# Kernel tuning notes

Measured on AMD Instinct MI355X. Metric: run time of the kernel, lower is better.

The kernel has to match this reference:

```python
import jax, jax.numpy as jnp
import numpy as np

B, L, H, R = 8, 8256, 768, 24  # L = 128*129/2 flattened token-pair positions


def setup_inputs() -> dict:
    key = jax.random.key(0)
    k1, k2, k3 = jax.random.split(key, 3)
    hidden_state = jax.random.normal(k1, (B, L, H), dtype=jnp.float32)
    # per-relation Linear(hidden_size, 3) weights, stacked: (R, 3, H), (R, 3)
    W = jax.random.normal(k2, (R, 3, H), dtype=jnp.float32) * 0.02
    b = jax.random.normal(k3, (R, 3), dtype=jnp.float32) * 0.02
    return {"hidden_state": hidden_state, "W": W, "b": b}


def reference(hidden_state, W, b):
    # Batched equivalent of the per-relation Linear loop + stack(dim=1):
    # logits[b, r, l, t] = sum_h hidden_state[b,l,h] * W[r,t,h] + b[r,t]
    logits = jnp.einsum('blh,rth->brlt', hidden_state, W) + b[None, :, None, :]
    return jax.nn.softmax(logits, axis=-1)  # (B, R, L, 3)
```

## Files before the change

kernel.cpp:

```cpp
#include <hip/hip_runtime.h>


#define HD     768
#define LSEQ   8256
#define RREL   24
#define KSTEPS 24
#define NT     5
#define NCOL   72

typedef float f32x4 __attribute__((ext_vector_type(4)));
typedef short s16x8 __attribute__((ext_vector_type(8)));
typedef int   i32x4 __attribute__((ext_vector_type(4)));

__device__ __forceinline__ unsigned f2bf(float f) {
  unsigned u = __builtin_bit_cast(unsigned, f);
  u += 0x7FFFu + ((u >> 16) & 1u);
  return u >> 16;
}
__device__ __forceinline__ int pack2(float lo, float hi) {
  return (int)(f2bf(lo) | (f2bf(hi) << 16));
}

__global__ void conv_w_kernel(const float* __restrict__ W,
                              unsigned short* __restrict__ wsB) {
  int idx = blockIdx.x * 256 + threadIdx.x;
  if (idx >= KSTEPS * NT * 64) return;
  int ks   = idx / (NT * 64);
  int rem  = idx - ks * (NT * 64);
  int nt   = rem >> 6;
  int lane = rem & 63;
  int col  = nt * 16 + (lane & 15);
  int k0   = ks * 32 + (lane >> 4) * 8;
  unsigned short v[8] = {0, 0, 0, 0, 0, 0, 0, 0};
  if (col < NCOL) {
    const float* p = W + (size_t)col * HD + k0;
    float4 a = *(const float4*)p;
    float4 b = *(const float4*)(p + 4);
    v[0] = (unsigned short)f2bf(a.x); v[1] = (unsigned short)f2bf(a.y);
    v[2] = (unsigned short)f2bf(a.z); v[3] = (unsigned short)f2bf(a.w);
    v[4] = (unsigned short)f2bf(b.x); v[5] = (unsigned short)f2bf(b.y);
    v[6] = (unsigned short)f2bf(b.z); v[7] = (unsigned short)f2bf(b.w);
  }
  *(s16x8*)(wsB + (size_t)idx * 8) = *(s16x8*)v;
}

#define ALOAD(ks) do { if ((ks) < KSTEPS) {                        \
    abuf[(ks) % 3][0] = *(const float4*)(pA + (ks) * 32);          \
    abuf[(ks) % 3][1] = *(const float4*)(pA + (ks) * 32 + 4);      \
  } } while (0)

#define BLOAD_WS(ks) do { if ((ks) < KSTEPS) {                     \
    _Pragma("unroll")                                              \
    for (int nt_ = 0; nt_ < NT; ++nt_)                             \
      bbuf[(ks) & 1][nt_] = pWS[(ks) * NT * 64 + nt_ * 64 + lane]; \
  } } while (0)

#define BLOAD_FB(ks) do { if ((ks) < KSTEPS) {                     \
    _Pragma("unroll")                                              \
    for (int nt_ = 0; nt_ < 4; ++nt_) {                            \
      fbf[(ks) & 1][nt_][0] = *(const float4*)(pB[nt_] + (ks)*32); \
      fbf[(ks) & 1][nt_][1] = *(const float4*)(pB[nt_] + (ks)*32 + 4); \
    }                                                              \
    if (b4ok) {                                                    \
      fbf[(ks) & 1][4][0] = *(const float4*)(pB[4] + (ks)*32);     \
      fbf[(ks) & 1][4][1] = *(const float4*)(pB[4] + (ks)*32 + 4); \
    } else {                                                       \
      fbf[(ks) & 1][4][0] = make_float4(0.f,0.f,0.f,0.f);          \
      fbf[(ks) & 1][4][1] = make_float4(0.f,0.f,0.f,0.f);          \
    }                                                              \
  } } while (0)

template <bool USE_WS>
__global__ __launch_bounds__(256, 4)
void tagging_main(const float* __restrict__ hs, const float* __restrict__ W,
                  const float* __restrict__ bias,
                  const i32x4* __restrict__ pWS, float* __restrict__ out) {
  __shared__ float lg[4][16][84];

  const int lane = threadIdx.x & 63;
  const int wid  = threadIdx.x >> 6;
  const int m0   = (blockIdx.x * 4 + wid) * 16;

  const float* pA = hs + (size_t)(m0 + (lane >> 2)) * HD + (lane & 3) * 8;
  const int bp = ((lane & 15) * 4 + (lane >> 4)) * 4;

  const float* pB[NT];
  #pragma unroll
  for (int nt = 0; nt < NT; ++nt)
    pB[nt] = W + (size_t)(nt * 16 + (lane & 15)) * HD + (lane >> 4) * 8;
  const bool b4ok = (lane & 15) < 8;

  f32x4  acc[NT] = {};
  float4 abuf[3][2];
  i32x4  bbuf[2][NT];
  float4 fbf[2][NT][2];

  ALOAD(0); ALOAD(1);
  if constexpr (USE_WS) { BLOAD_WS(0); } else { BLOAD_FB(0); }

  #pragma unroll
  for (int ks = 0; ks < KSTEPS; ++ks) {
    ALOAD(ks + 2);
    if constexpr (USE_WS) { BLOAD_WS(ks + 1); } else { BLOAD_FB(ks + 1); }

    float4 a0 = abuf[ks % 3][0], a1 = abuf[ks % 3][1];
    int d0 = pack2(a0.x, a0.y), d1 = pack2(a0.z, a0.w);
    int d2 = pack2(a1.x, a1.y), d3 = pack2(a1.z, a1.w);
    i32x4 av;
    av[0] = __builtin_amdgcn_ds_bpermute(bp, d0);
    av[1] = __builtin_amdgcn_ds_bpermute(bp, d1);
    av[2] = __builtin_amdgcn_ds_bpermute(bp, d2);
    av[3] = __builtin_amdgcn_ds_bpermute(bp, d3);
    s16x8 af = __builtin_bit_cast(s16x8, av);

    #pragma unroll
    for (int nt = 0; nt < NT; ++nt) {
      s16x8 bf;
      if constexpr (USE_WS) {
        bf = __builtin_bit_cast(s16x8, bbuf[ks & 1][nt]);
      } else {
        float4 b0 = fbf[ks & 1][nt][0], b1 = fbf[ks & 1][nt][1];
        i32x4 bv;
        bv[0] = pack2(b0.x, b0.y); bv[1] = pack2(b0.z, b0.w);
        bv[2] = pack2(b1.x, b1.y); bv[3] = pack2(b1.z, b1.w);
        bf = __builtin_bit_cast(s16x8, bv);
      }
      acc[nt] = __builtin_amdgcn_mfma_f32_16x16x32_bf16(af, bf, acc[nt], 0, 0, 0);
    }
  }

  #pragma unroll
  for (int nt = 0; nt < NT; ++nt)
    #pragma unroll
    for (int j = 0; j < 4; ++j)
      lg[wid][(lane >> 4) * 4 + j][nt * 16 + (lane & 15)] = acc[nt][j];
  __syncthreads();

  #pragma unroll
  for (int it = 0; it < 6; ++it) {
    int flat = it * 64 + lane;
    int g    = flat >> 4;
    int tokl = flat & 15;
    unsigned tok = (unsigned)(m0 + tokl);
    unsigned b   = tok / LSEQ;
    unsigned l   = tok - b * LSEQ;
    float x0 = lg[wid][tokl][3 * g + 0] + bias[3 * g + 0];
    float x1 = lg[wid][tokl][3 * g + 1] + bias[3 * g + 1];
    float x2 = lg[wid][tokl][3 * g + 2] + bias[3 * g + 2];
    float mx = fmaxf(x0, fmaxf(x1, x2));
    float e0 = __expf(x0 - mx), e1 = __expf(x1 - mx), e2 = __expf(x2 - mx);
    float inv = 1.0f / (e0 + e1 + e2);
    size_t o = ((size_t)(b * RREL + g) * LSEQ + l) * 3;
    out[o + 0] = e0 * inv;
    out[o + 1] = e1 * inv;
    out[o + 2] = e2 * inv;
  }
}

extern "C" void kernel_launch(void* const* d_in, const int* in_sizes, int n_in,
                              void* d_out, int out_size, void* d_ws, size_t ws_size,
                              hipStream_t stream) {
  (void)in_sizes; (void)n_in; (void)out_size;
  const float* hs   = (const float*)d_in[0];
  const float* W    = (const float*)d_in[1];
  const float* bias = (const float*)d_in[2];
  float* out = (float*)d_out;

  const size_t needB = (size_t)KSTEPS * NT * 64 * 8 * 2;
  if (d_ws && ws_size >= needB) {
    hipLaunchKernelGGL(conv_w_kernel, dim3(30), dim3(256), 0, stream,
                       W, (unsigned short*)d_ws);
    hipLaunchKernelGGL((tagging_main<true>), dim3(1032), dim3(256), 0, stream,
                       hs, W, bias, (const i32x4*)d_ws, out);
  } else {
    hipLaunchKernelGGL((tagging_main<false>), dim3(1032), dim3(256), 0, stream,
                       hs, W, bias, nullptr, out);
  }
}
```

Measured before the change: 52.64 us.

## Use single-wave blocks computing two 16-row M tiles to reuse B fragments

Each block becomes one 64-thread wave that computes 32 tokens as two 16-row MFMA tiles, so every B fragment load feeds two MFMAs. The per-token batch division in the epilogue is hoisted to one per block, and the bf16 packing switches to the HIP intrinsic conversion. This roughly halves the weight-fragment traffic per token and drops the multi-wave block structure. In exchange it doubles accumulator and A-buffer registers, and with 64-thread blocks there may be fewer resident waves per CU.

```diff
diff --git a/kernel.cpp b/kernel.cpp
--- a/kernel.cpp
+++ b/kernel.cpp
@@ -1,4 +1,5 @@
 #include <hip/hip_runtime.h>
+#include <hip/hip_bf16.h>
 
 
 #define HD     768
@@ -12,13 +13,16 @@
 typedef short s16x8 __attribute__((ext_vector_type(8)));
 typedef int   i32x4 __attribute__((ext_vector_type(4)));
 
-__device__ __forceinline__ unsigned f2bf(float f) {
+__device__ __forceinline__ unsigned f2bf_rne(float f) {
   unsigned u = __builtin_bit_cast(unsigned, f);
   u += 0x7FFFu + ((u >> 16) & 1u);
   return u >> 16;
 }
+
 __device__ __forceinline__ int pack2(float lo, float hi) {
-  return (int)(f2bf(lo) | (f2bf(hi) << 16));
+  unsigned l = __bfloat16_as_ushort(__float2bfloat16(lo));
+  unsigned h = __bfloat16_as_ushort(__float2bfloat16(hi));
+  return (int)(l | (h << 16));
 }
 
 __global__ void conv_w_kernel(const float* __restrict__ W,
@@ -36,17 +40,20 @@
     const float* p = W + (size_t)col * HD + k0;
     float4 a = *(const float4*)p;
     float4 b = *(const float4*)(p + 4);
-    v[0] = (unsigned short)f2bf(a.x); v[1] = (unsigned short)f2bf(a.y);
-    v[2] = (unsigned short)f2bf(a.z); v[3] = (unsigned short)f2bf(a.w);
-    v[4] = (unsigned short)f2bf(b.x); v[5] = (unsigned short)f2bf(b.y);
-    v[6] = (unsigned short)f2bf(b.z); v[7] = (unsigned short)f2bf(b.w);
+    v[0] = (unsigned short)f2bf_rne(a.x); v[1] = (unsigned short)f2bf_rne(a.y);
+    v[2] = (unsigned short)f2bf_rne(a.z); v[3] = (unsigned short)f2bf_rne(a.w);
+    v[4] = (unsigned short)f2bf_rne(b.x); v[5] = (unsigned short)f2bf_rne(b.y);
+    v[6] = (unsigned short)f2bf_rne(b.z); v[7] = (unsigned short)f2bf_rne(b.w);
   }
   *(s16x8*)(wsB + (size_t)idx * 8) = *(s16x8*)v;
 }
 
 #define ALOAD(ks) do { if ((ks) < KSTEPS) {                        \
-    abuf[(ks) % 3][0] = *(const float4*)(pA + (ks) * 32);          \
-    abuf[(ks) % 3][1] = *(const float4*)(pA + (ks) * 32 + 4);      \
+    const int s_ = (ks) % 3, o_ = (ks) * 32;                       \
+    abuf[s_][0][0] = *(const float4*)(pA0 + o_);                   \
+    abuf[s_][0][1] = *(const float4*)(pA0 + o_ + 4);               \
+    abuf[s_][1][0] = *(const float4*)(pA1 + o_);                   \
+    abuf[s_][1][1] = *(const float4*)(pA1 + o_ + 4);               \
   } } while (0)
 
 #define BLOAD_WS(ks) do { if ((ks) < KSTEPS) {                     \
@@ -71,17 +78,17 @@
   } } while (0)
 
 template <bool USE_WS>
-__global__ __launch_bounds__(256, 4)
+__global__ __launch_bounds__(64, 2)
 void tagging_main(const float* __restrict__ hs, const float* __restrict__ W,
                   const float* __restrict__ bias,
                   const i32x4* __restrict__ pWS, float* __restrict__ out) {
-  __shared__ float lg[4][16][84];
+  __shared__ float lg[32][85];
 
-  const int lane = threadIdx.x & 63;
-  const int wid  = threadIdx.x >> 6;
-  const int m0   = (blockIdx.x * 4 + wid) * 16;
+  const int lane = threadIdx.x;
+  const int m0   = blockIdx.x * 32;
 
-  const float* pA = hs + (size_t)(m0 + (lane >> 2)) * HD + (lane & 3) * 8;
+  const float* pA0 = hs + (size_t)(m0 + (lane >> 2)) * HD + (lane & 3) * 8;
+  const float* pA1 = pA0 + 16 * HD;
   const int bp = ((lane & 15) * 4 + (lane >> 4)) * 4;
 
   const float* pB[NT];
@@ -90,8 +97,8 @@
     pB[nt] = W + (size_t)(nt * 16 + (lane & 15)) * HD + (lane >> 4) * 8;
   const bool b4ok = (lane & 15) < 8;
 
-  f32x4  acc[NT] = {};
-  float4 abuf[3][2];
+  f32x4  acc[2][NT] = {};
+  float4 abuf[3][2][2];
   i32x4  bbuf[2][NT];
   float4 fbf[2][NT][2];
 
@@ -103,15 +110,17 @@
     ALOAD(ks + 2);
     if constexpr (USE_WS) { BLOAD_WS(ks + 1); } else { BLOAD_FB(ks + 1); }
 
-    float4 a0 = abuf[ks % 3][0], a1 = abuf[ks % 3][1];
-    int d0 = pack2(a0.x, a0.y), d1 = pack2(a0.z, a0.w);
-    int d2 = pack2(a1.x, a1.y), d3 = pack2(a1.z, a1.w);
-    i32x4 av;
-    av[0] = __builtin_amdgcn_ds_bpermute(bp, d0);
-    av[1] = __builtin_amdgcn_ds_bpermute(bp, d1);
-    av[2] = __builtin_amdgcn_ds_bpermute(bp, d2);
-    av[3] = __builtin_amdgcn_ds_bpermute(bp, d3);
-    s16x8 af = __builtin_bit_cast(s16x8, av);
+    s16x8 af[2];
+    #pragma unroll
+    for (int mt = 0; mt < 2; ++mt) {
+      float4 a0 = abuf[ks % 3][mt][0], a1 = abuf[ks % 3][mt][1];
+      i32x4 av;
+      av[0] = __builtin_amdgcn_ds_bpermute(bp, pack2(a0.x, a0.y));
+      av[1] = __builtin_amdgcn_ds_bpermute(bp, pack2(a0.z, a0.w));
+      av[2] = __builtin_amdgcn_ds_bpermute(bp, pack2(a1.x, a1.y));
+      av[3] = __builtin_amdgcn_ds_bpermute(bp, pack2(a1.z, a1.w));
+      af[mt] = __builtin_bit_cast(s16x8, av);
+    }
 
     #pragma unroll
     for (int nt = 0; nt < NT; ++nt) {
@@ -125,32 +134,34 @@
         bv[2] = pack2(b1.x, b1.y); bv[3] = pack2(b1.z, b1.w);
         bf = __builtin_bit_cast(s16x8, bv);
       }
-      acc[nt] = __builtin_amdgcn_mfma_f32_16x16x32_bf16(af, bf, acc[nt], 0, 0, 0);
+      acc[0][nt] = __builtin_amdgcn_mfma_f32_16x16x32_bf16(af[0], bf, acc[0][nt], 0, 0, 0);
+      acc[1][nt] = __builtin_amdgcn_mfma_f32_16x16x32_bf16(af[1], bf, acc[1][nt], 0, 0, 0);
     }
   }
 
   #pragma unroll
-  for (int nt = 0; nt < NT; ++nt)
+  for (int mt = 0; mt < 2; ++mt)
     #pragma unroll
-    for (int j = 0; j < 4; ++j)
-      lg[wid][(lane >> 4) * 4 + j][nt * 16 + (lane & 15)] = acc[nt][j];
+    for (int nt = 0; nt < NT; ++nt)
+      #pragma unroll
+      for (int j = 0; j < 4; ++j)
+        lg[mt * 16 + (lane >> 4) * 4 + j][nt * 16 + (lane & 15)] = acc[mt][nt][j];
   __syncthreads();
 
+  const int bidx = m0 / LSEQ;
+  const int l0   = m0 - bidx * LSEQ;
   #pragma unroll
-  for (int it = 0; it < 6; ++it) {
+  for (int it = 0; it < 12; ++it) {
     int flat = it * 64 + lane;
-    int g    = flat >> 4;
-    int tokl = flat & 15;
-    unsigned tok = (unsigned)(m0 + tokl);
-    unsigned b   = tok / LSEQ;
-    unsigned l   = tok - b * LSEQ;
-    float x0 = lg[wid][tokl][3 * g + 0] + bias[3 * g + 0];
-    float x1 = lg[wid][tokl][3 * g + 1] + bias[3 * g + 1];
-    float x2 = lg[wid][tokl][3 * g + 2] + bias[3 * g + 2];
+    int g    = flat >> 5;
+    int tokl = flat & 31;
+    float x0 = lg[tokl][3 * g + 0] + bias[3 * g + 0];
+    float x1 = lg[tokl][3 * g + 1] + bias[3 * g + 1];
+    float x2 = lg[tokl][3 * g + 2] + bias[3 * g + 2];
     float mx = fmaxf(x0, fmaxf(x1, x2));
     float e0 = __expf(x0 - mx), e1 = __expf(x1 - mx), e2 = __expf(x2 - mx);
     float inv = 1.0f / (e0 + e1 + e2);
-    size_t o = ((size_t)(b * RREL + g) * LSEQ + l) * 3;
+    size_t o = ((size_t)(bidx * RREL + g) * LSEQ + l0 + tokl) * 3;
     out[o + 0] = e0 * inv;
     out[o + 1] = e1 * inv;
     out[o + 2] = e2 * inv;
@@ -170,10 +181,10 @@
   if (d_ws && ws_size >= needB) {
     hipLaunchKernelGGL(conv_w_kernel, dim3(30), dim3(256), 0, stream,
                        W, (unsigned short*)d_ws);
-    hipLaunchKernelGGL((tagging_main<true>), dim3(1032), dim3(256), 0, stream,
+    hipLaunchKernelGGL((tagging_main<true>), dim3(2064), dim3(64), 0, stream,
                        hs, W, bias, (const i32x4*)d_ws, out);
   } else {
-    hipLaunchKernelGGL((tagging_main<false>), dim3(1032), dim3(256), 0, stream,
+    hipLaunchKernelGGL((tagging_main<false>), dim3(2064), dim3(64), 0, stream,
                        hs, W, bias, nullptr, out);
   }
 }
```

After: 46.64 us. 11.4% less time.
